# Optimization experiments

Hardware: AMD Instinct MI355X
Metric: run time of the kernel (lower is better)

## Reference

```python
import jax, jax.numpy as jnp
import numpy as np

D_MODEL = 2048
H_TOTAL = 32
D_HEAD = D_MODEL // H_TOTAL  # 64
H_ACTIVE = 4
ROPE_BASE = 10000.0


def _apply_rope(t, cos, sin):
    # t: [B, H, T, DH]; cos/sin: [T, DH//2]; interleaved pair rotation
    t1 = t[..., 0::2]
    t2 = t[..., 1::2]
    r1 = t1 * cos - t2 * sin
    r2 = t1 * sin + t2 * cos
    return jnp.stack([r1, r2], axis=-1).reshape(t.shape)


def setup_inputs() -> dict:
    key = jax.random.key(0)
    ks = jax.random.split(key, 4)
    x = jax.random.normal(ks[0], (4, 1024, D_MODEL), dtype=jnp.float32)
    w_router = jax.random.normal(ks[1], (D_MODEL, H_TOTAL), dtype=jnp.float32) * 0.02
    w_qkv = jax.random.normal(ks[2], (D_MODEL, 3 * D_MODEL), dtype=jnp.float32) * 0.02
    w_out = jax.random.normal(ks[3], (D_MODEL, D_MODEL), dtype=jnp.float32) * 0.02
    return {"x": x, "w_router": w_router, "w_qkv": w_qkv, "w_out": w_out}


def reference(x, w_router, w_qkv, w_out):
    B, T, _ = x.shape
    # --- SwitchRouter: per-token probabilities over heads ---
    probs = jax.nn.softmax(x @ w_router, axis=-1)            # [B, T, H]
    # top-h_active heads per token (dense-math equivalent of sparse dispatch)
    _, top_idx = jax.lax.top_k(probs, H_ACTIVE)              # [B, T, HA]
    mask = jnp.sum(jax.nn.one_hot(top_idx, H_TOTAL, dtype=x.dtype), axis=-2)  # [B, T, H]
    gate = probs * mask                                      # router-scored gate

    # --- QKV projection ---
    qkv = x @ w_qkv                                          # [B, T, 3D]
    q, k, v = jnp.split(qkv, 3, axis=-1)
    def to_heads(t):
        return t.reshape(B, T, H_TOTAL, D_HEAD).transpose(0, 2, 1, 3)  # [B, H, T, DH]
    q, k, v = to_heads(q), to_heads(k), to_heads(v)

    # --- RoPE ---
    inv_freq = 1.0 / (ROPE_BASE ** (jnp.arange(0, D_HEAD, 2, dtype=jnp.float32) / D_HEAD))
    ang = jnp.arange(T, dtype=jnp.float32)[:, None] * inv_freq[None, :]  # [T, DH/2]
    cos, sin = jnp.cos(ang), jnp.sin(ang)
    q = _apply_rope(q, cos, sin)
    k = _apply_rope(k, cos, sin)

    # --- causal SDPA ---
    scores = jnp.einsum('bhqd,bhkd->bhqk', q, k) / np.float32(np.sqrt(D_HEAD))
    causal = jnp.tril(jnp.ones((T, T), dtype=bool))
    scores = jnp.where(causal, scores, jnp.finfo(scores.dtype).min)
    attn = jax.nn.softmax(scores, axis=-1)
    out = jnp.einsum('bhqk,bhkd->bhqd', attn, v)             # [B, H, T, DH]

    # --- gate: only active heads contribute (scatter-back equivalent) ---
    out = out * gate.transpose(0, 2, 1)[..., None]           # [B, H, T, DH]
    out = out.transpose(0, 2, 1, 3).reshape(B, T, D_MODEL)
    return out @ w_out
```

## Files before the change

kernel.cpp:

```cpp
#include <hip/hip_runtime.h>
#include <hip/hip_bf16.h>
#include <stdint.h>
#include <stddef.h>

typedef __attribute__((ext_vector_type(8))) short bf16x8;
typedef __attribute__((ext_vector_type(8))) unsigned short u16x8;
typedef __attribute__((ext_vector_type(4))) float f32x4;
typedef __attribute__((ext_vector_type(16))) float f32x16;

#define TT 1024

__device__ __forceinline__ unsigned short f2bf(float f){
  unsigned u = __builtin_bit_cast(unsigned, f);
  unsigned r = 0x7fffu + ((u >> 16) & 1u);
  return (unsigned short)((u + r) >> 16);
}
__device__ __forceinline__ float bf2f(unsigned short s){
  unsigned u = ((unsigned)s) << 16;
  return __builtin_bit_cast(float, u);
}
__device__ __forceinline__ void gload16(const unsigned short* g, unsigned short* l){
  __builtin_amdgcn_global_load_lds(
      (const __attribute__((address_space(1))) void*)g,
      (__attribute__((address_space(3))) void*)l, 16, 0, 0);
}

#define MFMA32(a, b, c) __builtin_amdgcn_mfma_f32_32x32x16_bf16((a), (b), (c), 0, 0, 0)
#define MFMA_B16(a, b, c) __builtin_amdgcn_mfma_f32_16x16x32_bf16((a), (b), (c), 0, 0, 0)

__global__ __launch_bounds__(256) void prep2_kernel(const float* __restrict__ x,
                                                    const float* __restrict__ wr,
                                                    const float* __restrict__ wqkv,
                                                    const float* __restrict__ wout,
                                                    unsigned short* __restrict__ x_bf,
                                                    float* __restrict__ gate,
                                                    unsigned char* __restrict__ heads4,
                                                    float* __restrict__ tab,
                                                    unsigned short* __restrict__ wqkvT,
                                                    unsigned short* __restrict__ woutT){
  __shared__ float xc[8 * 256];
  __shared__ float red[8 * 8 * 32];
  __shared__ float tile[32][33];
  const int tid = threadIdx.x;

  if (blockIdx.x >= 512){
    int tb = blockIdx.x - 512;
    int bx = tb & 255, by = tb >> 8;
    const float* in; unsigned short* out; int C;
    if (bx < 192){ in = wqkv; out = wqkvT; C = 6144; }
    else         { in = wout; out = woutT; C = 2048; bx -= 192; }
    const int R = 2048;
    int c0 = bx * 32, r0 = by * 32;
    int tx = tid & 31, ty = tid >> 5;
    for (int i = ty; i < 32; i += 8)
      tile[i][tx] = in[(size_t)(r0 + i) * C + c0 + tx];
    __syncthreads();
    for (int i = ty; i < 32; i += 8)
      out[(size_t)(c0 + i) * R + r0 + tx] = f2bf(tile[tx][i]);
    return;
  }

  const int tok0 = blockIdx.x * 8;
  const int p = tid >> 5, h = tid & 31;

  if (blockIdx.x < 128){
    int i2 = blockIdx.x * 256 + tid;
    int pos = i2 >> 5, ii = i2 & 31;
    float freq = powf(10000.0f, -(float)ii / 32.0f);
    float ang = (float)pos * freq;
    tab[i2 * 2]     = cosf(ang);
    tab[i2 * 2 + 1] = sinf(ang);
  }

  float acc[8] = {0.f,0.f,0.f,0.f,0.f,0.f,0.f,0.f};
  for (int kb = 0; kb < 8; kb++){
    __syncthreads();
    {
      int tok = tid >> 5, e = (tid & 31) * 8;
      const float* xp = x + (size_t)(tok0 + tok) * 2048 + kb * 256 + e;
      float4 v0 = *(const float4*)xp, v1 = *(const float4*)(xp + 4);
      float vals[8] = {v0.x, v0.y, v0.z, v0.w, v1.x, v1.y, v1.z, v1.w};
      u16x8 ob;
      #pragma unroll
      for (int jj = 0; jj < 8; jj++) ob[jj] = f2bf(vals[jj]);
      *(u16x8*)(x_bf + (size_t)(tok0 + tok) * 2048 + kb * 256 + e) = ob;
      #pragma unroll
      for (int jj = 0; jj < 8; jj++) xc[tok * 256 + e + jj] = vals[jj];
    }
    __syncthreads();
    const float* wp = wr + (size_t)(kb * 256 + p * 32) * 32 + h;
    #pragma unroll 4
    for (int j = 0; j < 32; j++){
      float wv = wp[j * 32];
      #pragma unroll
      for (int tok = 0; tok < 8; tok++)
        acc[tok] += xc[tok * 256 + p * 32 + j] * wv;
    }
  }
  #pragma unroll
  for (int tok = 0; tok < 8; tok++) red[(p * 8 + tok) * 32 + h] = acc[tok];
  __syncthreads();
  {
    int lane = tid & 63;
    int tok = (tid >> 6) * 2 + (lane >> 5);
    int hh = lane & 31;
    float logit = 0.f;
    #pragma unroll
    for (int pp = 0; pp < 8; pp++) logit += red[(pp * 8 + tok) * 32 + hh];
    float m = logit;
    #pragma unroll
    for (int s = 16; s >= 1; s >>= 1) m = fmaxf(m, __shfl_xor(m, s));
    float e = __expf(logit - m);
    float sum = e;
    #pragma unroll
    for (int s = 16; s >= 1; s >>= 1) sum += __shfl_xor(sum, s);
    float prob = e / sum;
    float v = logit; int sel = 0;
    #pragma unroll
    for (int rr2 = 0; rr2 < 4; rr2++){
      float bv = v; int bi = hh;
      #pragma unroll
      for (int s = 16; s >= 1; s >>= 1){
        float ov = __shfl_xor(bv, s); int oi = __shfl_xor(bi, s);
        if (ov > bv || (ov == bv && oi < bi)) { bv = ov; bi = oi; }
      }
      if (hh == bi) { sel = 1; v = -3.4e38f; }
    }
    gate[(size_t)(tok0 + tok) * 32 + hh] = sel ? prob : 0.f;
    unsigned long long bal = __ballot(sel != 0);
    unsigned selmask = (unsigned)(bal >> ((lane >> 5) * 32));
    if (sel){
      int r = __popc(selmask & ((1u << hh) - 1u));
      heads4[(size_t)(tok0 + tok) * 4 + r] = (unsigned char)hh;
    }
  }
}

__global__ void compact_kernel(const unsigned char* __restrict__ heads4,
                               unsigned short* __restrict__ idx, int* __restrict__ counts){
  int bh = blockIdx.x;
  int b = bh >> 5, h = bh & 31;
  int lane = threadIdx.x;
  int base = 0;
  for (int c = 0; c < 16; c++){
    int t = c * 64 + lane;
    unsigned u = ((const unsigned*)heads4)[b * 1024 + t];
    int r = -1;
    if (((u      ) & 255) == (unsigned)h) r = 0;
    else if (((u >>  8) & 255) == (unsigned)h) r = 1;
    else if (((u >> 16) & 255) == (unsigned)h) r = 2;
    else if (((u >> 24) & 255) == (unsigned)h) r = 3;
    bool act = (r >= 0);
    unsigned long long mask = __ballot(act);
    int pos = base + __popcll(mask & ((1ull << lane) - 1ull));
    if (act) idx[bh * 1024 + pos] = (unsigned short)(t | (r << 10));
    base += __popcll(mask);
  }
  if (lane == 0) counts[bh] = base;
}

__global__ __launch_bounds__(256) void qgemm_kernel(const unsigned short* __restrict__ x_bf,
                                                    const unsigned short* __restrict__ wqkvT,
                                                    const unsigned short* __restrict__ idx,
                                                    const int* __restrict__ counts,
                                                    const float* __restrict__ tab,
                                                    unsigned short* __restrict__ qact){
  __shared__ float red[4][64][64];
  const int bh = blockIdx.x, qt = blockIdx.y;
  const int count = counts[bh];
  if (qt * 64 >= count) return;
  const int b = bh >> 5, h = bh & 31;
  const int tid = threadIdx.x, lane = tid & 63, w = tid >> 6;
  const int li = lane & 15, lg = lane >> 4;
  const int nvalid = min(64, count - qt * 64);
  const unsigned short* myidx = idx + bh * 1024 + qt * 64;

  int atok[4];
  #pragma unroll
  for (int ai = 0; ai < 4; ai++){
    int s = ai * 16 + li;
    atok[ai] = (s < nvalid) ? (myidx[s] & 1023) : 0;
  }
  const unsigned short* Bbase = wqkvT + (size_t)(h * 64) * 2048;

  f32x4 acc[4][4];
  #pragma unroll
  for (int i = 0; i < 4; i++)
    #pragma unroll
    for (int j = 0; j < 4; j++) acc[i][j] = f32x4{0.f, 0.f, 0.f, 0.f};

  const int k0w = w * 512;
  #pragma unroll 2
  for (int ks = 0; ks < 16; ks++){
    int k0 = k0w + ks * 32 + lg * 8;
    bf16x8 af[4], bw[4];
    #pragma unroll
    for (int ai = 0; ai < 4; ai++)
      af[ai] = *(const bf16x8*)(x_bf + (size_t)(b * 1024 + atok[ai]) * 2048 + k0);
    #pragma unroll
    for (int ni = 0; ni < 4; ni++)
      bw[ni] = *(const bf16x8*)(Bbase + (size_t)(ni * 16 + li) * 2048 + k0);
    #pragma unroll
    for (int ai = 0; ai < 4; ai++)
      #pragma unroll
      for (int ni = 0; ni < 4; ni++)
        acc[ai][ni] = MFMA_B16(af[ai], bw[ni], acc[ai][ni]);
  }
  #pragma unroll
  for (int ai = 0; ai < 4; ai++)
    #pragma unroll
    for (int ni = 0; ni < 4; ni++)
      #pragma unroll
      for (int rr = 0; rr < 4; rr++)
        red[w][ai * 16 + lg * 4 + rr][ni * 16 + li] = acc[ai][ni][rr];
  __syncthreads();

  int q = tid >> 2, dbase = (tid & 3) * 16;
  if (q < nvalid){
    int e = myidx[q];
    int tok = e & 1023, r = e >> 10;
    unsigned short* op = qact + ((size_t)((b << 10) + tok) * 4 + r) * 64;
    const float* tp = tab + ((size_t)tok * 32 + (dbase >> 1)) * 2;
    #pragma unroll
    for (int p = 0; p < 8; p++){
      int d0 = dbase + 2 * p;
      float v0 = red[0][q][d0] + red[1][q][d0] + red[2][q][d0] + red[3][q][d0];
      float v1 = red[0][q][d0 + 1] + red[1][q][d0 + 1] + red[2][q][d0 + 1] + red[3][q][d0 + 1];
      float c = tp[2 * p], s = tp[2 * p + 1];
      op[d0]     = f2bf(v0 * c - v1 * s);
      op[d0 + 1] = f2bf(v0 * s + v1 * c);
    }
  }
}

__global__ __launch_bounds__(256, 2) void gemmk(const unsigned short* __restrict__ A,
                                                const unsigned short* __restrict__ Bt,
                                                unsigned short* __restrict__ kbuf,
                                                unsigned short* __restrict__ vt,
                                                const float* __restrict__ tab,
                                                int K, int nbm){
  extern __shared__ unsigned short smem[];
  constexpr int MREP = 4;
  constexpr int BM = MREP * 64;
  constexpr int AU = MREP * 2048;
  constexpr int SLOT = AU + 4096;
  const int nblk = gridDim.x;
  const int raw = blockIdx.x;
  const int tile = (raw & 7) * (nblk >> 3) + (raw >> 3);
  const int bn = tile / nbm, bm = tile % nbm;

  const int tid = threadIdx.x, lane = tid & 63, wid = tid >> 6;
  const int wrow = wid >> 1, wcol = wid & 1;
  const int l31 = lane & 31, hi = lane >> 5;
  const int X = ((l31 >> 1) & 7) << 4;

  const unsigned short* gA[MREP];
  const unsigned short* gB[2];
  #pragma unroll
  for (int p = 0; p < MREP; p++){
    int L = tid * 16 + p * 4096;
    int line = L >> 7;
    int cs = (L & 127) ^ ((line & 7) << 4);
    gA[p] = A + (size_t)(bm * BM + line * 2 + (cs >> 6)) * K + ((cs & 63) >> 1);
  }
  #pragma unroll
  for (int p = 0; p < 2; p++){
    int L = tid * 16 + p * 4096;
    int line = L >> 7;
    int cs = (L & 127) ^ ((line & 7) << 4);
    gB[p] = Bt + (size_t)(bn * 128 + line * 2 + (cs >> 6)) * K + ((cs & 63) >> 1);
  }

  f32x16 acc[MREP][2];
  #pragma unroll
  for (int i = 0; i < MREP; i++)
    #pragma unroll
    for (int j = 0; j < 2; j++) acc[i][j] = f32x16{0,0,0,0,0,0,0,0,0,0,0,0,0,0,0,0};

  const int NT = K >> 5;
  #pragma unroll
  for (int tt = 0; tt < 2; tt++){
    unsigned short* sb = smem + tt * SLOT;
    #pragma unroll
    for (int p = 0; p < MREP; p++) gload16(gA[p] + (size_t)tt * 32, sb + tid * 8 + p * 2048);
    #pragma unroll
    for (int p = 0; p < 2; p++)    gload16(gB[p] + (size_t)tt * 32, sb + AU + tid * 8 + p * 2048);
  }

  for (int t = 0; t < NT; ++t){
    if (t < NT - 1) asm volatile("s_waitcnt vmcnt(6)" ::: "memory");
    else            asm volatile("s_waitcnt vmcnt(0)" ::: "memory");
    __builtin_amdgcn_s_barrier();
    __builtin_amdgcn_sched_barrier(0);
    const unsigned short* bs = smem + (t % 3) * SLOT;
    unsigned short* ns = smem + ((t + 2) % 3) * SLOT;
    const bool st = (t + 2 < NT);
    #pragma unroll
    for (int ks = 0; ks < 2; ks++){
      const int bo = (((l31 & 1) * 64 + ks * 32 + hi * 16) ^ X) >> 1;
      bf16x8 av[MREP], bv[2];
      #pragma unroll
      for (int i = 0; i < MREP; i++)
        av[i] = *(const bf16x8*)(bs + (wrow * (MREP * 16) + i * 16 + (l31 >> 1)) * 64 + bo);
      #pragma unroll
      for (int j = 0; j < 2; j++)
        bv[j] = *(const bf16x8*)(bs + AU + (wcol * 32 + j * 16 + (l31 >> 1)) * 64 + bo);
      if (st){
        if (ks == 0){
          #pragma unroll
          for (int p = 0; p < 3; p++)
            gload16(gA[p] + (size_t)(t + 2) * 32, ns + tid * 8 + p * 2048);
        } else {
          gload16(gA[3] + (size_t)(t + 2) * 32, ns + tid * 8 + 3 * 2048);
          #pragma unroll
          for (int p = 0; p < 2; p++)
            gload16(gB[p] + (size_t)(t + 2) * 32, ns + AU + tid * 8 + p * 2048);
        }
      }
      #pragma unroll
      for (int i = 0; i < MREP; i++){
        acc[i][0] = MFMA32(av[i], bv[0], acc[i][0]);
        acc[i][1] = MFMA32(av[i], bv[1], acc[i][1]);
      }
    }
  }

  if (bn < 16){
    #pragma unroll
    for (int i = 0; i < MREP; i++){
      #pragma unroll
      for (int j = 0; j < 2; j++){
        int col = bn * 128 + wcol * 64 + j * 32 + l31;
        int ii = (col & 63) >> 1;
        #pragma unroll
        for (int g = 0; g < 4; g++){
          #pragma unroll
          for (int rr = 0; rr < 4; rr++){
            int row = bm * BM + wrow * (BM / 2) + i * 32 + g * 8 + hi * 4 + rr;
            int pos = row & (TT - 1);
            const float* tp = tab + ((size_t)pos * 32 + ii) * 2;
            float c = tp[0], s = tp[1];
            float val = acc[i][j][g * 4 + rr];
            float pv = __shfl_xor(val, 1);
            float res = (lane & 1) ? (pv * s + val * c) : (val * c - pv * s);
            kbuf[(size_t)row * 2048 + col] = f2bf(res);
          }
        }
      }
    }
  } else {
    #pragma unroll
    for (int i = 0; i < MREP; i++){
      #pragma unroll
      for (int j = 0; j < 2; j++){
        int vcol = bn * 128 + wcol * 64 + j * 32 + l31 - 2048;
        int hh = vcol >> 6, d = vcol & 63;
        int row0 = bm * BM + wrow * (BM / 2) + i * 32 + hi * 4;
        int b = row0 >> 10, t0 = row0 & (TT - 1);
        #pragma unroll
        for (int g = 0; g < 4; g++){
          ushort4 pk;
          pk.x = f2bf(acc[i][j][g * 4 + 0]); pk.y = f2bf(acc[i][j][g * 4 + 1]);
          pk.z = f2bf(acc[i][j][g * 4 + 2]); pk.w = f2bf(acc[i][j][g * 4 + 3]);
          *(ushort4*)(vt + ((size_t)((b * 32 + hh) * 64 + d)) * TT + t0 + g * 8) = pk;
        }
      }
    }
  }
}

__global__ __launch_bounds__(256) void attn_sparse_kernel(unsigned short* __restrict__ qact,
                                                          const unsigned short* __restrict__ kbuf,
                                                          const unsigned short* __restrict__ vt,
                                                          const float* __restrict__ gate,
                                                          const unsigned short* __restrict__ idx,
                                                          const int* __restrict__ counts){
  __shared__ unsigned short Ks[64 * 64];
  __shared__ unsigned short Vs[64 * 64];
  __shared__ unsigned short Ps[4][16 * 64];
  const int bh = blockIdx.x, qt = blockIdx.y;
  const int count = counts[bh];
  if (qt * 64 >= count) return;
  const int b = bh >> 5, h = bh & 31;
  const int tid = threadIdx.x, lane = tid & 63, w = tid >> 6;
  const int li = lane & 15, lg = lane >> 4;
  const unsigned short* myidx = idx + bh * 1024 + qt * 64;
  const int nvalid = min(64, count - qt * 64);
  const int qmax = myidx[nvalid - 1] & 1023;

  int qi[4];
  #pragma unroll
  for (int r = 0; r < 4; r++){
    int s = w * 16 + lg * 4 + r;
    qi[r] = (s < nvalid) ? (myidx[s] & 1023) : -1;
  }
  bf16x8 qf0, qf1;
  {
    int s = w * 16 + li;
    int e2 = (s < nvalid) ? myidx[s] : 0;
    const unsigned short* qp = qact + ((size_t)((b << 10) + (e2 & 1023)) * 4 + (e2 >> 10)) * 64;
    qf0 = *(const bf16x8*)(qp + lg * 8);
    qf1 = *(const bf16x8*)(qp + 32 + lg * 8);
  }
  f32x4 o[4];
  #pragma unroll
  for (int i = 0; i < 4; i++) o[i] = f32x4{0.f, 0.f, 0.f, 0.f};
  float m_run[4], l_run[4];
  #pragma unroll
  for (int r = 0; r < 4; r++){ m_run[r] = -1e30f; l_run[r] = 0.f; }

  const int nkt = (qmax >> 6) + 1;
  for (int kt = 0; kt < nkt; kt++){
    const int kb = kt * 64;
    #pragma unroll
    for (int s2 = 0; s2 < 2; s2++){
      int s = s2 * 256 + tid;
      int r = s >> 3, c = (s & 7) * 8;
      gload16(kbuf + (size_t)(b * TT + kb + r) * 2048 + h * 64 + c, &Ks[s * 8]);
      gload16(vt + (size_t)(bh * 64 + r) * TT + kb + c, &Vs[s * 8]);
    }
    __syncthreads();

    f32x4 s4[4];
    #pragma unroll
    for (int ni = 0; ni < 4; ni++){
      bf16x8 k0 = *(const bf16x8*)(&Ks[(ni * 16 + li) * 64 + lg * 8]);
      bf16x8 k1 = *(const bf16x8*)(&Ks[(ni * 16 + li) * 64 + 32 + lg * 8]);
      f32x4 t = f32x4{0.f, 0.f, 0.f, 0.f};
      t = MFMA_B16(qf0, k0, t);
      t = MFMA_B16(qf1, k1, t);
      s4[ni] = t;
    }
    float mt[4];
    #pragma unroll
    for (int r = 0; r < 4; r++) mt[r] = -1e30f;
    #pragma unroll
    for (int ni = 0; ni < 4; ni++){
      int kidx = kb + ni * 16 + li;
      #pragma unroll
      for (int r = 0; r < 4; r++){
        float val = s4[ni][r] * 0.125f;
        val = (kidx <= qi[r]) ? val : -1e30f;
        s4[ni][r] = val;
        mt[r] = fmaxf(mt[r], val);
      }
    }
    #pragma unroll
    for (int r = 0; r < 4; r++){
      #pragma unroll
      for (int sh = 8; sh >= 1; sh >>= 1) mt[r] = fmaxf(mt[r], __shfl_xor(mt[r], sh));
      float mnew = fmaxf(m_run[r], mt[r]);
      float corr = __expf(m_run[r] - mnew);
      m_run[r] = mnew;
      l_run[r] *= corr;
      #pragma unroll
      for (int j = 0; j < 4; j++) o[j][r] *= corr;
    }
    float rs[4] = {0.f, 0.f, 0.f, 0.f};
    #pragma unroll
    for (int ni = 0; ni < 4; ni++)
      #pragma unroll
      for (int r = 0; r < 4; r++){
        float p = __expf(s4[ni][r] - m_run[r]);
        s4[ni][r] = p;
        rs[r] += p;
      }
    #pragma unroll
    for (int r = 0; r < 4; r++){
      #pragma unroll
      for (int sh = 8; sh >= 1; sh >>= 1) rs[r] += __shfl_xor(rs[r], sh);
      l_run[r] += rs[r];
    }
    #pragma unroll
    for (int ni = 0; ni < 4; ni++)
      #pragma unroll
      for (int r = 0; r < 4; r++)
        Ps[w][(lg * 4 + r) * 64 + ni * 16 + li] = f2bf(s4[ni][r]);
    #pragma unroll
    for (int ks = 0; ks < 2; ks++){
      bf16x8 pa = *(const bf16x8*)(&Ps[w][li * 64 + ks * 32 + lg * 8]);
      #pragma unroll
      for (int ni = 0; ni < 4; ni++){
        bf16x8 vb = *(const bf16x8*)(&Vs[(ni * 16 + li) * 64 + ks * 32 + lg * 8]);
        o[ni] = MFMA_B16(pa, vb, o[ni]);
      }
    }
    __syncthreads();
  }
  #pragma unroll
  for (int r = 0; r < 4; r++){
    if (qi[r] < 0) continue;
    float g = gate[(size_t)(b * TT + qi[r]) * 32 + h];
    float inv = g / l_run[r];
    int e = myidx[w * 16 + lg * 4 + r];
    unsigned short* op = qact + ((size_t)((b << 10) + (e & 1023)) * 4 + (e >> 10)) * 64;
    #pragma unroll
    for (int ni = 0; ni < 4; ni++)
      op[ni * 16 + li] = f2bf(o[ni][r] * inv);
  }
}

__global__ __launch_bounds__(256) void outsp_kernel(const unsigned short* __restrict__ qact,
                                                    const unsigned short* __restrict__ woutT,
                                                    const unsigned short* __restrict__ idx,
                                                    const int* __restrict__ counts,
                                                    unsigned short* __restrict__ p0,
                                                    unsigned short* __restrict__ p1,
                                                    unsigned short* __restrict__ p2,
                                                    unsigned short* __restrict__ p3){
  __shared__ unsigned short As[64 * 64];
  __shared__ unsigned short sidx[64];
  const int bh = blockIdx.x, qt = blockIdx.y;
  const int count = counts[bh];
  if (qt * 64 >= count) return;
  const int b = bh >> 5, h = bh & 31;
  const int tid = threadIdx.x, lane = tid & 63, w = tid >> 6;
  const int li = lane & 15, lg = lane >> 4;
  const int nvalid = min(64, count - qt * 64);
  const unsigned short* myidx = idx + bh * 1024 + qt * 64;
  const int n0 = blockIdx.z * 256 + w * 64;

  bf16x8 bfr[4][2];
  #pragma unroll
  for (int ni = 0; ni < 4; ni++)
    #pragma unroll
    for (int kh = 0; kh < 2; kh++)
      bfr[ni][kh] = *(const bf16x8*)(woutT + (size_t)(n0 + ni * 16 + li) * 2048 + h * 64 + kh * 32 + lg * 8);

  if (tid < 64) sidx[tid] = myidx[(tid < nvalid) ? tid : 0];
  #pragma unroll
  for (int s2 = 0; s2 < 2; s2++){
    int s = s2 * 256 + tid;
    int row = s >> 3, bc = (s & 7) * 16;
    int e = myidx[(row < nvalid) ? row : 0];
    const unsigned short* src = qact + ((size_t)((b << 10) + (e & 1023)) * 4 + (e >> 10)) * 64;
    gload16(src + ((bc ^ ((row & 7) << 4)) >> 1), &As[s * 8]);
  }
  __syncthreads();

  const int kX = (li & 7) << 4;
  f32x4 acc[4][4];
  #pragma unroll
  for (int i = 0; i < 4; i++)
    #pragma unroll
    for (int j = 0; j < 4; j++) acc[i][j] = f32x4{0.f, 0.f, 0.f, 0.f};
  #pragma unroll
  for (int ti = 0; ti < 4; ti++){
    bf16x8 a0 = *(const bf16x8*)(&As[((ti * 16 + li) * 128 + ((lg * 16) ^ kX)) >> 1]);
    bf16x8 a1 = *(const bf16x8*)(&As[((ti * 16 + li) * 128 + ((64 + lg * 16) ^ kX)) >> 1]);
    #pragma unroll
    for (int ni = 0; ni < 4; ni++){
      acc[ti][ni] = MFMA_B16(a0, bfr[ni][0], acc[ti][ni]);
      acc[ti][ni] = MFMA_B16(a1, bfr[ni][1], acc[ti][ni]);
    }
  }
  #pragma unroll
  for (int ti = 0; ti < 4; ti++){
    #pragma unroll
    for (int rr = 0; rr < 4; rr++){
      int slot = ti * 16 + lg * 4 + rr;
      if (slot < nvalid){
        int e = sidx[slot];
        int tok = e & 1023, rk = e >> 10;
        unsigned short* pp = (rk == 0) ? p0 : (rk == 1) ? p1 : (rk == 2) ? p2 : p3;
        size_t base = (size_t)(b * 1024 + tok) * 2048 + n0;
        #pragma unroll
        for (int ni = 0; ni < 4; ni++)
          pp[base + ni * 16 + li] = f2bf(acc[ti][ni][rr]);
      }
    }
  }
}

__global__ void reduce_kernel(const unsigned short* __restrict__ p0,
                              const unsigned short* __restrict__ p1,
                              const unsigned short* __restrict__ p2,
                              const unsigned short* __restrict__ p3,
                              float* __restrict__ out){
  size_t i = ((size_t)blockIdx.x * 256 + threadIdx.x) * 8;
  u16x8 a = *(const u16x8*)(p0 + i);
  u16x8 b = *(const u16x8*)(p1 + i);
  u16x8 c = *(const u16x8*)(p2 + i);
  u16x8 d = *(const u16x8*)(p3 + i);
  #pragma unroll
  for (int j = 0; j < 8; j++)
    out[i + j] = bf2f(a[j]) + bf2f(b[j]) + bf2f(c[j]) + bf2f(d[j]);
}

extern "C" void kernel_launch(void* const* d_in, const int* in_sizes, int n_in,
                              void* d_out, int out_size, void* d_ws, size_t ws_size,
                              hipStream_t stream){
  const float* x        = (const float*)d_in[0];
  const float* w_router = (const float*)d_in[1];
  const float* w_qkv    = (const float*)d_in[2];
  const float* w_out    = (const float*)d_in[3];
  float* out = (float*)d_out;
  char* ws = (char*)d_ws;

  unsigned short* kbuf   = (unsigned short*)(ws);
  unsigned short* vt     = (unsigned short*)(ws + 16777216);
  unsigned short* qact   = (unsigned short*)(ws + 33554432);
  unsigned short* idx    = (unsigned short*)(ws + 37748736);
  int* counts            = (int*)(ws + 38010880);
  unsigned char* heads4  = (unsigned char*)(ws + 38011392);
  unsigned short* x_bf   = (unsigned short*)(ws + 50331648);
  unsigned short* wqkvT  = (unsigned short*)(ws + 67108864);
  unsigned short* woutT  = (unsigned short*)(ws + 92274688);
  float* gate            = (float*)(ws + 100663296);
  float* tab             = (float*)(ws + 101187584);
  unsigned short* part0  = kbuf;
  unsigned short* part1  = vt;
  unsigned short* part2  = x_bf;
  unsigned short* part3  = wqkvT;

  constexpr int KV_LDS = 73728;
  (void)hipFuncSetAttribute(reinterpret_cast<const void*>(&gemmk),
                            hipFuncAttributeMaxDynamicSharedMemorySize, KV_LDS);

  hipLaunchKernelGGL(prep2_kernel, dim3(16896), dim3(256), 0, stream,
                     x, w_router, w_qkv, w_out, x_bf, gate, heads4, tab, wqkvT, woutT);
  hipLaunchKernelGGL(compact_kernel, dim3(128), dim3(64), 0, stream, heads4, idx, counts);
  hipLaunchKernelGGL(gemmk, dim3(512), dim3(256), KV_LDS, stream,
                     x_bf, wqkvT + (size_t)2048 * 2048, kbuf, vt, tab, 2048, 16);
  hipLaunchKernelGGL(qgemm_kernel, dim3(128, 16), dim3(256), 0, stream,
                     x_bf, wqkvT, idx, counts, tab, qact);
  hipLaunchKernelGGL(attn_sparse_kernel, dim3(128, 16), dim3(256), 0, stream,
                     qact, kbuf, vt, gate, idx, counts);
  hipLaunchKernelGGL(outsp_kernel, dim3(128, 16, 8), dim3(256), 0, stream,
                     qact, woutT, idx, counts, part0, part1, part2, part3);
  hipLaunchKernelGGL(reduce_kernel, dim3(4096), dim3(256), 0, stream,
                     part0, part1, part2, part3, out);
}
```

Before: 241.5 us.

## Load K/V and gathered activation fragments directly from global memory instead of LDS

In the sparse attention kernel, the K and V tiles are no longer staged through shared memory with block barriers. Each wave now reads its MFMA fragments straight from global memory. The out-projection kernel likewise drops the swizzled LDS staging of the gathered activation rows and loads them per-wave from global through the index table. This removes LDS traffic and __syncthreads, but the four waves now fetch the same K/V data redundantly, relying on cache, with less coalesced access patterns.

```diff
diff --git a/kernel.cpp b/kernel.cpp
--- a/kernel.cpp
+++ b/kernel.cpp
@@ -375,8 +375,6 @@
                                                           const float* __restrict__ gate,
                                                           const unsigned short* __restrict__ idx,
                                                           const int* __restrict__ counts){
-  __shared__ unsigned short Ks[64 * 64];
-  __shared__ unsigned short Vs[64 * 64];
   __shared__ unsigned short Ps[4][16 * 64];
   const int bh = blockIdx.x, qt = blockIdx.y;
   const int count = counts[bh];
@@ -409,23 +407,18 @@
   #pragma unroll
   for (int r = 0; r < 4; r++){ m_run[r] = -1e30f; l_run[r] = 0.f; }
 
+  const unsigned short* kbase = kbuf + (size_t)(b * TT) * 2048 + h * 64;
+  const unsigned short* vbase = vt + (size_t)(bh * 64) * TT;
+
   const int nkt = (qmax >> 6) + 1;
   for (int kt = 0; kt < nkt; kt++){
     const int kb = kt * 64;
-    #pragma unroll
-    for (int s2 = 0; s2 < 2; s2++){
-      int s = s2 * 256 + tid;
-      int r = s >> 3, c = (s & 7) * 8;
-      gload16(kbuf + (size_t)(b * TT + kb + r) * 2048 + h * 64 + c, &Ks[s * 8]);
-      gload16(vt + (size_t)(bh * 64 + r) * TT + kb + c, &Vs[s * 8]);
-    }
-    __syncthreads();
-
     f32x4 s4[4];
     #pragma unroll
     for (int ni = 0; ni < 4; ni++){
-      bf16x8 k0 = *(const bf16x8*)(&Ks[(ni * 16 + li) * 64 + lg * 8]);
-      bf16x8 k1 = *(const bf16x8*)(&Ks[(ni * 16 + li) * 64 + 32 + lg * 8]);
+      const unsigned short* kp = kbase + (size_t)(kb + ni * 16 + li) * 2048;
+      bf16x8 k0 = *(const bf16x8*)(kp + lg * 8);
+      bf16x8 k1 = *(const bf16x8*)(kp + 32 + lg * 8);
       f32x4 t = f32x4{0.f, 0.f, 0.f, 0.f};
       t = MFMA_B16(qf0, k0, t);
       t = MFMA_B16(qf1, k1, t);
@@ -481,11 +474,10 @@
       bf16x8 pa = *(const bf16x8*)(&Ps[w][li * 64 + ks * 32 + lg * 8]);
       #pragma unroll
       for (int ni = 0; ni < 4; ni++){
-        bf16x8 vb = *(const bf16x8*)(&Vs[(ni * 16 + li) * 64 + ks * 32 + lg * 8]);
+        bf16x8 vb = *(const bf16x8*)(vbase + (size_t)(ni * 16 + li) * TT + kb + ks * 32 + lg * 8);
         o[ni] = MFMA_B16(pa, vb, o[ni]);
       }
     }
-    __syncthreads();
   }
   #pragma unroll
   for (int r = 0; r < 4; r++){
@@ -508,7 +500,6 @@
                                                     unsigned short* __restrict__ p1,
                                                     unsigned short* __restrict__ p2,
                                                     unsigned short* __restrict__ p3){
-  __shared__ unsigned short As[64 * 64];
   __shared__ unsigned short sidx[64];
   const int bh = blockIdx.x, qt = blockIdx.y;
   const int count = counts[bh];
@@ -528,17 +519,8 @@
       bfr[ni][kh] = *(const bf16x8*)(woutT + (size_t)(n0 + ni * 16 + li) * 2048 + h * 64 + kh * 32 + lg * 8);
 
   if (tid < 64) sidx[tid] = myidx[(tid < nvalid) ? tid : 0];
-  #pragma unroll
-  for (int s2 = 0; s2 < 2; s2++){
-    int s = s2 * 256 + tid;
-    int row = s >> 3, bc = (s & 7) * 16;
-    int e = myidx[(row < nvalid) ? row : 0];
-    const unsigned short* src = qact + ((size_t)((b << 10) + (e & 1023)) * 4 + (e >> 10)) * 64;
-    gload16(src + ((bc ^ ((row & 7) << 4)) >> 1), &As[s * 8]);
-  }
   __syncthreads();
 
-  const int kX = (li & 7) << 4;
   f32x4 acc[4][4];
   #pragma unroll
   for (int i = 0; i < 4; i++)
@@ -546,8 +528,10 @@
     for (int j = 0; j < 4; j++) acc[i][j] = f32x4{0.f, 0.f, 0.f, 0.f};
   #pragma unroll
   for (int ti = 0; ti < 4; ti++){
-    bf16x8 a0 = *(const bf16x8*)(&As[((ti * 16 + li) * 128 + ((lg * 16) ^ kX)) >> 1]);
-    bf16x8 a1 = *(const bf16x8*)(&As[((ti * 16 + li) * 128 + ((64 + lg * 16) ^ kX)) >> 1]);
+    int e = sidx[ti * 16 + li];
+    const unsigned short* ap = qact + ((size_t)((b << 10) + (e & 1023)) * 4 + (e >> 10)) * 64;
+    bf16x8 a0 = *(const bf16x8*)(ap + lg * 8);
+    bf16x8 a1 = *(const bf16x8*)(ap + 32 + lg * 8);
     #pragma unroll
     for (int ni = 0; ni < 4; ni++){
       acc[ti][ni] = MFMA_B16(a0, bfr[ni][0], acc[ti][ni]);
```

Result: slower. 265.2 us (+9.8%).
